# Optimization experiments

Hardware: AMD Instinct MI355X
Metric: run time of the kernel (lower is better)

Reference implementation:

```python
import jax, jax.numpy as jnp
import numpy as np

DIM = 96
D_STATE = 16
D_CONV = 3
D_INNER = 192   # int(DIM * 2.0)
DT_RANK = 6     # ceil(DIM / 16)
K = 4           # cross-scan directions
BATCH, H, W = 2, 56, 56


def setup_inputs() -> dict:
    key = jax.random.key(0)
    k = jax.random.split(key, 8)
    x = jax.random.normal(k[0], (BATCH, DIM, H, W), jnp.float32)
    W_in = jax.random.normal(k[1], (DIM, 2 * D_INNER), jnp.float32) / np.sqrt(DIM)
    W_conv = jax.random.normal(k[2], (D_INNER, 1, D_CONV, D_CONV), jnp.float32) / D_CONV
    b_conv = jnp.zeros((D_INNER,), jnp.float32)
    W_xproj = jax.random.normal(k[3], (K, D_INNER, DT_RANK + 2 * D_STATE), jnp.float32) / np.sqrt(D_INNER)
    W_dt = jax.random.normal(k[4], (K, DT_RANK, D_INNER), jnp.float32) / np.sqrt(DT_RANK)
    # dt bias init as in torch: dt ~ exp(U * (log 0.1 - log 0.001) + log 0.001), inv-softplus
    dt = jnp.exp(jax.random.uniform(k[5], (K, D_INNER), jnp.float32)
                 * (np.log(0.1) - np.log(0.001)) + np.log(0.001))
    dt = jnp.clip(dt, 1e-4, None)
    b_dt = dt + jnp.log(-jnp.expm1(-dt))
    A_logs = jnp.log(jnp.broadcast_to(jnp.arange(1, D_STATE + 1, dtype=jnp.float32),
                                      (K, D_INNER, D_STATE)))
    Ds = jnp.ones((K, D_INNER), jnp.float32)
    W_out = jax.random.normal(k[6], (D_INNER, DIM), jnp.float32) / np.sqrt(D_INNER)
    return dict(x=x, W_in=W_in, W_conv=W_conv, b_conv=b_conv, W_xproj=W_xproj,
                W_dt=W_dt, b_dt=b_dt, A_logs=A_logs, Ds=Ds, W_out=W_out)


def _ss2d(x, W_in, W_conv, b_conv, W_xproj, W_dt, b_dt, A_logs, Ds, W_out):
    Bsz, C, Hh, Ww = x.shape
    L = Hh * Ww
    # in_proj
    xf = x.transpose(0, 2, 3, 1).reshape(Bsz, L, C)        # (B, L, C)
    xz = xf @ W_in
    xp, z = jnp.split(xz, 2, axis=-1)                       # each (B, L, D)
    # depthwise conv + silu
    xi = xp.reshape(Bsz, Hh, Ww, -1).transpose(0, 3, 1, 2)  # (B, D, H, W)
    pad = D_CONV // 2
    xi = jax.lax.conv_general_dilated(
        xi, W_conv, (1, 1), ((pad, pad), (pad, pad)),
        feature_group_count=xi.shape[1],
        dimension_numbers=('NCHW', 'OIHW', 'NCHW')) + b_conv[None, :, None, None]
    xi = jax.nn.silu(xi)
    D = xi.shape[1]
    # cross-scan: 4 directions, each (B, L, D)
    x1 = xi.reshape(Bsz, D, L).transpose(0, 2, 1)
    x2 = xi[:, :, :, ::-1].reshape(Bsz, D, L).transpose(0, 2, 1)
    xt = xi.transpose(0, 1, 3, 2)                           # (B, D, W, H)
    x3 = xt.reshape(Bsz, D, L).transpose(0, 2, 1)
    x4 = xt[:, :, :, ::-1].reshape(Bsz, D, L).transpose(0, 2, 1)
    xs = jnp.stack([x1, x2, x3, x4])                        # (K, B, L, D)
    # per-direction projections, batched over K
    xdbl = jnp.einsum('kbld,kde->kble', xs, W_xproj)
    dr = xdbl[..., :DT_RANK]
    Bk = xdbl[..., DT_RANK:DT_RANK + D_STATE]               # (K, B, L, N)
    Ck = xdbl[..., DT_RANK + D_STATE:]                      # (K, B, L, N)
    delta = jax.nn.softplus(jnp.einsum('kblr,krd->kbld', dr, W_dt)
                            + b_dt[:, None, None, :])       # (K, B, L, D)
    A = -jnp.exp(A_logs)                                    # (K, D, N)

    def step(h, inp):
        x_i, d_i, B_i, C_i = inp  # (K,B,D), (K,B,D), (K,B,N), (K,B,N)
        dA = jnp.exp(d_i[..., None] * A[:, None])           # (K, B, D, N)
        h = dA * h + (d_i * x_i)[..., None] * B_i[:, :, None, :]
        y = jnp.einsum('kbdn,kbn->kbd', h, C_i)
        return h, y

    h0 = jnp.zeros((K, Bsz, D, D_STATE), xs.dtype)
    seq = (xs.transpose(2, 0, 1, 3), delta.transpose(2, 0, 1, 3),
           Bk.transpose(2, 0, 1, 3), Ck.transpose(2, 0, 1, 3))
    _, ys = jax.lax.scan(step, h0, seq)                     # (L, K, B, D)
    ys = ys.transpose(1, 2, 0, 3) + xs * Ds[:, None, None, :]  # (K, B, L, D)
    # cross-merge back to row-major (h w) order
    y1 = ys[0]
    y2 = ys[1].reshape(Bsz, Hh, Ww, D)[:, :, ::-1, :].reshape(Bsz, L, D)
    y3 = ys[2].reshape(Bsz, Ww, Hh, D).transpose(0, 2, 1, 3).reshape(Bsz, L, D)
    y4 = ys[3].reshape(Bsz, Ww, Hh, D)[:, :, ::-1, :].transpose(0, 2, 1, 3).reshape(Bsz, L, D)
    y = (y1 + y2 + y3 + y4) * jax.nn.silu(z)
    out = (y @ W_out).reshape(Bsz, Hh, Ww, C).transpose(0, 3, 1, 2)
    return out


def reference(x, W_in, W_conv, b_conv, W_xproj, W_dt, b_dt, A_logs, Ds, W_out):
    return _ss2d(x, W_in, W_conv, b_conv, W_xproj, W_dt, b_dt, A_logs, Ds, W_out)
```

## Files before the change

kernel.cpp:

```cpp
#include <hip/hip_runtime.h>
#include <math.h>

constexpr int BATCH  = 2;
constexpr int CDIM   = 96;
constexpr int HH     = 56;
constexpr int WW     = 56;
constexpr int LL     = HH * WW;
constexpr int DIN    = 192;
constexpr int NK     = 4;
constexpr int NST    = 16;
constexpr int RNK    = 6;
constexpr int EPROJ  = RNK + 2 * NST;
constexpr int SCH    = 64;
constexpr int NCH    = LL / SCH;
constexpr int CGRP   = DIN / 16;

constexpr size_t SZ_PX   = (size_t)BATCH * LL * DIN;
constexpr size_t OFF_XP  = 0;
constexpr size_t OFF_Z   = OFF_XP + SZ_PX;
constexpr size_t OFF_XI  = OFF_Z  + SZ_PX;
constexpr size_t OFF_DL  = OFF_XI + SZ_PX;
constexpr size_t SZ_DL   = (size_t)NK * BATCH * LL * DIN;
constexpr size_t OFF_B   = OFF_DL + SZ_DL;
constexpr size_t SZ_BC   = (size_t)NK * BATCH * LL * NST;
constexpr size_t OFF_C   = OFF_B + SZ_BC;
constexpr size_t OFF_Y   = OFF_C + SZ_BC;
constexpr size_t SZ_HS   = (size_t)NK * BATCH * NCH * DIN * NST;
constexpr size_t OFF_HE  = OFF_Y + SZ_PX;
constexpr size_t OFF_HI  = OFF_HE + SZ_HS;

__device__ __forceinline__ float silu(float v) {
    return v / (1.0f + __expf(-v));
}

__device__ __forceinline__ float row_reduce16(float p) {
    p += __int_as_float(__builtin_amdgcn_update_dpp(0, __float_as_int(p), 0x128, 0xf, 0xf, true));
    p += __int_as_float(__builtin_amdgcn_update_dpp(0, __float_as_int(p), 0x124, 0xf, 0xf, true));
    p += __int_as_float(__builtin_amdgcn_update_dpp(0, __float_as_int(p), 0x122, 0xf, 0xf, true));
    p += __int_as_float(__builtin_amdgcn_update_dpp(0, __float_as_int(p), 0x121, 0xf, 0xf, true));
    return p;
}

__device__ __forceinline__ int seq_to_lr(int k, int l) {
    int q = l / WW;
    int r = l - q * WW;
    if (k == 0) return l;
    if (k == 1) return q * WW + (WW - 1 - r);
    if (k == 2) return r * WW + q;
    return (WW - 1 - r) * WW + q;
}

__device__ __forceinline__ int spatial_to_seq(int k, int s) {
    int h = s / WW;
    int w = s - h * WW;
    if (k == 0) return s;
    if (k == 1) return h * WW + (WW - 1 - w);
    if (k == 2) return w * WW + h;
    return w * WW + (WW - 1 - h);
}

__device__ __forceinline__ size_t hs_idx(int c, int kb, int d, int n) {
    return ((size_t)(c * (NK * BATCH) + kb) * DIN + d) * NST + n;
}

constexpr int K1_PIX = 8;
__global__ __launch_bounds__(384) void k_inproj(
        const float* __restrict__ x, const float* __restrict__ W_in,
        float* __restrict__ xp, float* __restrict__ z) {
    __shared__ float sx[K1_PIX][100];
    int gp0 = blockIdx.x * K1_PIX;
    int t   = threadIdx.x;
    int b   = gp0 / LL;
    int l0  = gp0 - b * LL;
    for (int i = t; i < K1_PIX * CDIM; i += 384) {
        int p = i % K1_PIX;
        int c = i / K1_PIX;
        sx[p][c] = x[((size_t)(b * CDIM + c)) * LL + l0 + p];
    }
    __syncthreads();
    int e = t;
    float acc[K1_PIX];
#pragma unroll
    for (int p = 0; p < K1_PIX; p++) acc[p] = 0.0f;
    for (int c = 0; c < CDIM; c++) {
        float w = W_in[c * (2 * DIN) + e];
#pragma unroll
        for (int p = 0; p < K1_PIX; p++) acc[p] = fmaf(sx[p][c], w, acc[p]);
    }
    if (e < DIN) {
#pragma unroll
        for (int p = 0; p < K1_PIX; p++)
            xp[((size_t)(gp0 + p)) * DIN + e] = acc[p];
    } else {
        int e2 = e - DIN;
#pragma unroll
        for (int p = 0; p < K1_PIX; p++)
            z[((size_t)(gp0 + p)) * DIN + e2] = acc[p];
    }
}

__global__ __launch_bounds__(192) void k_conv(
        const float* __restrict__ xp, const float* __restrict__ Wc,
        const float* __restrict__ bc, float* __restrict__ xi) {
    int gp = blockIdx.x;
    int d  = threadIdx.x;
    int b  = gp / LL;
    int l  = gp - b * LL;
    int h  = l / WW;
    int w  = l - h * WW;
    float acc = bc[d];
#pragma unroll
    for (int dy = -1; dy <= 1; dy++) {
        int hh = h + dy;
        if (hh < 0 || hh >= HH) continue;
#pragma unroll
        for (int dx = -1; dx <= 1; dx++) {
            int ww = w + dx;
            if (ww < 0 || ww >= WW) continue;
            acc = fmaf(xp[((size_t)b * LL + hh * WW + ww) * DIN + d],
                       Wc[d * 9 + (dy + 1) * 3 + (dx + 1)], acc);
        }
    }
    xi[(size_t)gp * DIN + d] = silu(acc);
}

constexpr int K3_PIX = 16;
__global__ __launch_bounds__(256) void k_xproj(
        const float* __restrict__ xi, const float* __restrict__ W_xproj,
        const float* __restrict__ W_dt, const float* __restrict__ b_dt,
        const float* __restrict__ Ds,
        float* __restrict__ dbuf, float* __restrict__ Bbuf,
        float* __restrict__ Cbuf, float* __restrict__ ysum) {
    __shared__ float v[K3_PIX][DIN];
    __shared__ float drs[K3_PIX][RNK];
    int k   = blockIdx.y;
    int gp0 = blockIdx.x * K3_PIX;
    int b   = gp0 / LL;
    int l0  = gp0 - b * LL;
    int t   = threadIdx.x;
    for (int i = t; i < K3_PIX * DIN; i += 256) {
        int p = i / DIN, d = i % DIN;
        v[p][d] = xi[((size_t)(gp0 + p)) * DIN + d];
    }
    __syncthreads();
    for (int i = t; i < K3_PIX * EPROJ; i += 256) {
        int p = i / EPROJ, e = i % EPROJ;
        const float* wp = W_xproj + (size_t)k * DIN * EPROJ + e;
        float acc = 0.0f;
        for (int d = 0; d < DIN; d++) acc = fmaf(v[p][d], wp[d * EPROJ], acc);
        int ls = spatial_to_seq(k, l0 + p);
        size_t base = ((size_t)(k * BATCH + b)) * LL + ls;
        if (e < RNK)            drs[p][e] = acc;
        else if (e < RNK + NST) Bbuf[base * NST + (e - RNK)] = acc;
        else                    Cbuf[base * NST + (e - RNK - NST)] = acc;
    }
    __syncthreads();
    for (int i = t; i < K3_PIX * DIN; i += 256) {
        int p = i / DIN, d = i % DIN;
        float acc = b_dt[k * DIN + d];
#pragma unroll
        for (int r = 0; r < RNK; r++)
            acc = fmaf(drs[p][r], W_dt[((size_t)k * RNK + r) * DIN + d], acc);
        float sp = (acc > 20.0f) ? acc : log1pf(__expf(acc));
        int ls = spatial_to_seq(k, l0 + p);
        dbuf[(((size_t)(k * BATCH + b)) * LL + ls) * DIN + d] = sp;
        if (k == 0) {
            float dsum = Ds[d] + Ds[DIN + d] + Ds[2 * DIN + d] + Ds[3 * DIN + d];
            ysum[((size_t)(gp0 + p)) * DIN + d] = v[p][d] * dsum;
        }
    }
}

__global__ __launch_bounds__(256) void k_scanA(
        const float* __restrict__ xi, const float* __restrict__ dbuf,
        const float* __restrict__ Bbuf, const float* __restrict__ A_logs,
        float* __restrict__ Pbuf, float* __restrict__ hend) {
    __shared__ float2 sDU[SCH][16];
    __shared__ float  sB1[SCH][16];
    int c   = blockIdx.x;
    int blk = blockIdx.y;
    int k   = blk / (BATCH * CGRP);
    int rem = blk % (BATCH * CGRP);
    int b   = rem / CGRP;
    int cg  = rem % CGRP;
    int d0  = cg * 16;
    int t    = threadIdx.x;
    int lane = t & 63, wave = t >> 6;
    int grp  = lane >> 4, n = lane & 15;
    int ch   = wave * 4 + grp;
    int d    = d0 + ch;
    float A = -__expf(A_logs[((size_t)(k * DIN + d)) * NST + n]);
    size_t sbase = ((size_t)(k * BATCH + b)) * LL;
    const float* dp = dbuf + sbase * DIN + d0;
    const float* bp = Bbuf + sbase * NST;
    const float* up = xi   + (size_t)b * LL * DIN;
    int l0 = c * SCH;
    for (int i = t; i < SCH * 16; i += 256) {
        int s = i >> 4, cc = i & 15;
        int l = l0 + s;
        int lr = seq_to_lr(k, l);
        float dlt = dp[(size_t)l * DIN + cc];
        float u   = up[(size_t)lr * DIN + d0 + cc];
        sDU[s][cc] = make_float2(dlt, dlt * u);
        sB1[s][cc] = bp[(size_t)l * NST + cc];
    }
    __syncthreads();
    float h = 0.0f, P = 1.0f;
#pragma unroll 8
    for (int s = 0; s < SCH; s++) {
        float2 du = sDU[s][ch];
        float dA  = __expf(du.x * A);
        h = fmaf(dA, h, du.y * sB1[s][n]);
        P *= dA;
    }
    size_t idx = hs_idx(c, k * BATCH + b, d, n);
    Pbuf[idx] = P;
    hend[idx] = h;
}

__global__ __launch_bounds__(256) void k_scanB(
        const float* __restrict__ Pbuf, const float* __restrict__ hend,
        float* __restrict__ hin) {
    int tid = blockIdx.x * 256 + threadIdx.x;
    int kb  = tid / (DIN * NST);
    int dn  = tid % (DIN * NST);
    float h = 0.0f;
    for (int c = 0; c < NCH; c++) {
        size_t idx = ((size_t)(c * (NK * BATCH) + kb)) * (DIN * NST) + dn;
        hin[idx] = h;
        h = fmaf(Pbuf[idx], h, hend[idx]);
    }
}

__global__ __launch_bounds__(256) void k_scanC(
        const float* __restrict__ xi, const float* __restrict__ dbuf,
        const float* __restrict__ Bbuf, const float* __restrict__ Cbuf,
        const float* __restrict__ A_logs, const float* __restrict__ hin,
        float* __restrict__ ysum) {
    __shared__ float2 sDU[SCH][16];
    __shared__ float2 sBC[SCH][16];
    __shared__ float  sY[SCH][16];
    int c   = blockIdx.x;
    int blk = blockIdx.y;
    int k   = blk / (BATCH * CGRP);
    int rem = blk % (BATCH * CGRP);
    int b   = rem / CGRP;
    int cg  = rem % CGRP;
    int d0  = cg * 16;
    int t    = threadIdx.x;
    int lane = t & 63, wave = t >> 6;
    int grp  = lane >> 4, n = lane & 15;
    int ch   = wave * 4 + grp;
    int d    = d0 + ch;
    float A = -__expf(A_logs[((size_t)(k * DIN + d)) * NST + n]);
    size_t sbase = ((size_t)(k * BATCH + b)) * LL;
    const float* dp = dbuf + sbase * DIN + d0;
    const float* bp = Bbuf + sbase * NST;
    const float* cp = Cbuf + sbase * NST;
    const float* up = xi   + (size_t)b * LL * DIN;
    float*       yp = ysum + (size_t)b * LL * DIN;
    int l0 = c * SCH;
    for (int i = t; i < SCH * 16; i += 256) {
        int s = i >> 4, cc = i & 15;
        int l = l0 + s;
        int lr = seq_to_lr(k, l);
        float dlt = dp[(size_t)l * DIN + cc];
        float u   = up[(size_t)lr * DIN + d0 + cc];
        sDU[s][cc] = make_float2(dlt, dlt * u);
        sBC[s][cc] = make_float2(bp[(size_t)l * NST + cc],
                                 cp[(size_t)l * NST + cc]);
    }
    float h = hin[hs_idx(c, k * BATCH + b, d, n)];
    __syncthreads();
#pragma unroll 4
    for (int s = 0; s < SCH; s++) {
        float2 du = sDU[s][ch];
        float2 bc = sBC[s][n];
        float dA  = __expf(du.x * A);
        h = fmaf(dA, h, du.y * bc.x);
        float p = row_reduce16(h * bc.y);
        if (n == 0) sY[s][ch] = p;
    }
    __syncthreads();
    for (int i = t; i < SCH * 16; i += 256) {
        int s = i >> 4, cc = i & 15;
        int lr = seq_to_lr(k, l0 + s);
        atomicAdd(&yp[(size_t)lr * DIN + d0 + cc], sY[s][cc]);
    }
}

constexpr int K5_PIX = 8;
__global__ __launch_bounds__(192) void k_out(
        const float* __restrict__ ysum, const float* __restrict__ zbuf,
        const float* __restrict__ W_out, float* __restrict__ out) {
    __shared__ float g[K5_PIX][DIN];
    __shared__ float so[CDIM][K5_PIX];
    int gp0 = blockIdx.x * K5_PIX;
    int b   = gp0 / LL;
    int l0  = gp0 - b * LL;
    int t   = threadIdx.x;
    for (int i = t; i < K5_PIX * DIN; i += 192) {
        int p = i / DIN, dd = i % DIN;
        size_t idx = (size_t)(gp0 + p) * DIN + dd;
        g[p][dd] = ysum[idx] * silu(zbuf[idx]);
    }
    __syncthreads();
    int f    = t % CDIM;
    int half = t / CDIM;
    float acc[4] = {0.f, 0.f, 0.f, 0.f};
    for (int dd = 0; dd < DIN; dd++) {
        float wv = W_out[dd * CDIM + f];
#pragma unroll
        for (int p = 0; p < 4; p++)
            acc[p] = fmaf(g[half * 4 + p][dd], wv, acc[p]);
    }
#pragma unroll
    for (int p = 0; p < 4; p++) so[f][half * 4 + p] = acc[p];
    __syncthreads();
    for (int i = t; i < CDIM * K5_PIX; i += 192) {
        int f2 = i / K5_PIX, p2 = i % K5_PIX;
        out[((size_t)(b * CDIM + f2)) * LL + l0 + p2] = so[f2][p2];
    }
}

extern "C" void kernel_launch(void* const* d_in, const int* in_sizes, int n_in,
                              void* d_out, int out_size, void* d_ws, size_t ws_size,
                              hipStream_t stream) {
    const float* x       = (const float*)d_in[0];
    const float* W_in    = (const float*)d_in[1];
    const float* W_conv  = (const float*)d_in[2];
    const float* b_conv  = (const float*)d_in[3];
    const float* W_xproj = (const float*)d_in[4];
    const float* W_dt    = (const float*)d_in[5];
    const float* b_dt    = (const float*)d_in[6];
    const float* A_logs  = (const float*)d_in[7];
    const float* Ds      = (const float*)d_in[8];
    const float* W_out   = (const float*)d_in[9];
    float* out = (float*)d_out;
    float* ws  = (float*)d_ws;

    float* xp   = ws + OFF_XP;
    float* z    = ws + OFF_Z;
    float* xi   = ws + OFF_XI;
    float* dbuf = ws + OFF_DL;
    float* Bbuf = ws + OFF_B;
    float* Cbuf = ws + OFF_C;
    float* ysum = ws + OFF_Y;
    float* hend = ws + OFF_HE;
    float* hin  = ws + OFF_HI;
    float* Pbuf = xp;

    k_inproj<<<(BATCH * LL) / K1_PIX, 384, 0, stream>>>(x, W_in, xp, z);
    k_conv<<<BATCH * LL, DIN, 0, stream>>>(xp, W_conv, b_conv, xi);
    dim3 g3((BATCH * LL) / K3_PIX, NK);
    k_xproj<<<g3, 256, 0, stream>>>(xi, W_xproj, W_dt, b_dt, Ds, dbuf, Bbuf, Cbuf, ysum);
    dim3 gs(NCH, NK * BATCH * CGRP);
    k_scanA<<<gs, 256, 0, stream>>>(xi, dbuf, Bbuf, A_logs, Pbuf, hend);
    k_scanB<<<(NK * BATCH * DIN * NST) / 256, 256, 0, stream>>>(Pbuf, hend, hin);
    k_scanC<<<gs, 256, 0, stream>>>(xi, dbuf, Bbuf, Cbuf, A_logs, hin, ysum);
    k_out<<<(BATCH * LL) / K5_PIX, 192, 0, stream>>>(ysum, z, W_out, out);
}
```

Before: 244.7 us.

## Recompute delta in scan kernels from low-rank projection instead of materializing it

Instead of writing the full per-direction delta tensor (K*B*L*D floats) in the x-projection kernel, only the rank-6 intermediate is stored, padded to 8 floats per position. Both scan kernels recompute the dt projection and softplus on the fly from this buffer and W_dt. The x-projection is also rewritten to use a transposed weight copy, built by a new small kernel each call, with float4 loads and two outputs per thread. This removes most of the delta write and read traffic, at the cost of recomputing the projection twice and one extra kernel launch.

```diff
diff --git a/kernel.cpp b/kernel.cpp
--- a/kernel.cpp
+++ b/kernel.cpp
@@ -19,18 +19,24 @@
 constexpr size_t OFF_XP  = 0;
 constexpr size_t OFF_Z   = OFF_XP + SZ_PX;
 constexpr size_t OFF_XI  = OFF_Z  + SZ_PX;
-constexpr size_t OFF_DL  = OFF_XI + SZ_PX;
-constexpr size_t SZ_DL   = (size_t)NK * BATCH * LL * DIN;
-constexpr size_t OFF_B   = OFF_DL + SZ_DL;
+constexpr size_t OFF_DR  = OFF_XI + SZ_PX;
+constexpr size_t SZ_DR   = (size_t)NK * BATCH * LL * 8;
+constexpr size_t OFF_B   = OFF_DR + SZ_DR;
 constexpr size_t SZ_BC   = (size_t)NK * BATCH * LL * NST;
 constexpr size_t OFF_C   = OFF_B + SZ_BC;
 constexpr size_t OFF_Y   = OFF_C + SZ_BC;
 constexpr size_t SZ_HS   = (size_t)NK * BATCH * NCH * DIN * NST;
 constexpr size_t OFF_HE  = OFF_Y + SZ_PX;
 constexpr size_t OFF_HI  = OFF_HE + SZ_HS;
+constexpr size_t OFF_WT  = OFF_HI + SZ_HS;
+constexpr size_t SZ_WT   = (size_t)NK * EPROJ * DIN;
 
 __device__ __forceinline__ float silu(float v) {
     return v / (1.0f + __expf(-v));
+}
+
+__device__ __forceinline__ float softplus_f(float x) {
+    return (x > 20.0f) ? x : __logf(1.0f + __expf(x));
 }
 
 __device__ __forceinline__ float row_reduce16(float p) {
@@ -61,6 +67,17 @@
 
 __device__ __forceinline__ size_t hs_idx(int c, int kb, int d, int n) {
     return ((size_t)(c * (NK * BATCH) + kb) * DIN + d) * NST + n;
+}
+
+__global__ __launch_bounds__(256) void k_wt(
+        const float* __restrict__ W_xproj, float* __restrict__ Wt) {
+    int i = blockIdx.x * 256 + threadIdx.x;
+    if (i >= NK * DIN * EPROJ) return;
+    int k = i / (DIN * EPROJ);
+    int r = i % (DIN * EPROJ);
+    int d = r / EPROJ;
+    int e = r % EPROJ;
+    Wt[((size_t)k * EPROJ + e) * DIN + d] = W_xproj[i];
 }
 
 constexpr int K1_PIX = 8;
@@ -126,54 +143,62 @@
 
 constexpr int K3_PIX = 16;
 __global__ __launch_bounds__(256) void k_xproj(
-        const float* __restrict__ xi, const float* __restrict__ W_xproj,
-        const float* __restrict__ W_dt, const float* __restrict__ b_dt,
+        const float* __restrict__ xi, const float* __restrict__ Wt,
         const float* __restrict__ Ds,
-        float* __restrict__ dbuf, float* __restrict__ Bbuf,
+        float* __restrict__ drbuf, float* __restrict__ Bbuf,
         float* __restrict__ Cbuf, float* __restrict__ ysum) {
-    __shared__ float v[K3_PIX][DIN];
-    __shared__ float drs[K3_PIX][RNK];
+    __shared__ float4 sv[K3_PIX][48];
     int k   = blockIdx.y;
     int gp0 = blockIdx.x * K3_PIX;
     int b   = gp0 / LL;
     int l0  = gp0 - b * LL;
     int t   = threadIdx.x;
-    for (int i = t; i < K3_PIX * DIN; i += 256) {
-        int p = i / DIN, d = i % DIN;
-        v[p][d] = xi[((size_t)(gp0 + p)) * DIN + d];
-    }
-    __syncthreads();
-    for (int i = t; i < K3_PIX * EPROJ; i += 256) {
-        int p = i / EPROJ, e = i % EPROJ;
-        const float* wp = W_xproj + (size_t)k * DIN * EPROJ + e;
-        float acc = 0.0f;
-        for (int d = 0; d < DIN; d++) acc = fmaf(v[p][d], wp[d * EPROJ], acc);
+    const float4* xin = (const float4*)(xi + (size_t)gp0 * DIN);
+    for (int i = t; i < K3_PIX * 48; i += 256)
+        sv[i / 48][i % 48] = xin[i];
+    __syncthreads();
+    if (k == 0) {
+        const float* svf = (const float*)sv;
+        for (int i = t; i < K3_PIX * DIN; i += 256) {
+            int d = i % DIN;
+            float dsum = Ds[d] + Ds[DIN + d] + Ds[2 * DIN + d] + Ds[3 * DIN + d];
+            ysum[(size_t)gp0 * DIN + i] = svf[i] * dsum;
+        }
+    }
+    for (int item = t; item < K3_PIX * 19; item += 256) {
+        int p  = item / 19;
+        int e0 = 2 * (item % 19);
+        const float4* w0 = (const float4*)(Wt + ((size_t)k * EPROJ + e0) * DIN);
+        const float4* w1 = w0 + 48;
+        float a0 = 0.0f, a1 = 0.0f;
+#pragma unroll 8
+        for (int j = 0; j < 48; j++) {
+            float4 vv = sv[p][j];
+            float4 wa = w0[j];
+            float4 wb = w1[j];
+            a0 = fmaf(vv.x, wa.x, a0); a0 = fmaf(vv.y, wa.y, a0);
+            a0 = fmaf(vv.z, wa.z, a0); a0 = fmaf(vv.w, wa.w, a0);
+            a1 = fmaf(vv.x, wb.x, a1); a1 = fmaf(vv.y, wb.y, a1);
+            a1 = fmaf(vv.z, wb.z, a1); a1 = fmaf(vv.w, wb.w, a1);
+        }
         int ls = spatial_to_seq(k, l0 + p);
-        size_t base = ((size_t)(k * BATCH + b)) * LL + ls;
-        if (e < RNK)            drs[p][e] = acc;
-        else if (e < RNK + NST) Bbuf[base * NST + (e - RNK)] = acc;
-        else                    Cbuf[base * NST + (e - RNK - NST)] = acc;
-    }
-    __syncthreads();
-    for (int i = t; i < K3_PIX * DIN; i += 256) {
-        int p = i / DIN, d = i % DIN;
-        float acc = b_dt[k * DIN + d];
-#pragma unroll
-        for (int r = 0; r < RNK; r++)
-            acc = fmaf(drs[p][r], W_dt[((size_t)k * RNK + r) * DIN + d], acc);
-        float sp = (acc > 20.0f) ? acc : log1pf(__expf(acc));
-        int ls = spatial_to_seq(k, l0 + p);
-        dbuf[(((size_t)(k * BATCH + b)) * LL + ls) * DIN + d] = sp;
-        if (k == 0) {
-            float dsum = Ds[d] + Ds[DIN + d] + Ds[2 * DIN + d] + Ds[3 * DIN + d];
-            ysum[((size_t)(gp0 + p)) * DIN + d] = v[p][d] * dsum;
+        size_t kb   = (size_t)(k * BATCH + b);
+        size_t b8   = (kb * LL + ls) * 8;
+        size_t b16  = (kb * LL + ls) * NST;
+        if (e0 < RNK) {
+            drbuf[b8 + e0] = a0; drbuf[b8 + e0 + 1] = a1;
+        } else if (e0 < RNK + NST) {
+            Bbuf[b16 + e0 - RNK] = a0; Bbuf[b16 + e0 - RNK + 1] = a1;
+        } else {
+            Cbuf[b16 + e0 - RNK - NST] = a0; Cbuf[b16 + e0 - RNK - NST + 1] = a1;
         }
     }
 }
 
 __global__ __launch_bounds__(256) void k_scanA(
-        const float* __restrict__ xi, const float* __restrict__ dbuf,
+        const float* __restrict__ xi, const float* __restrict__ drbuf,
         const float* __restrict__ Bbuf, const float* __restrict__ A_logs,
+        const float* __restrict__ W_dt, const float* __restrict__ b_dt,
         float* __restrict__ Pbuf, float* __restrict__ hend) {
     __shared__ float2 sDU[SCH][16];
     __shared__ float  sB1[SCH][16];
@@ -190,17 +215,31 @@
     int ch   = wave * 4 + grp;
     int d    = d0 + ch;
     float A = -__expf(A_logs[((size_t)(k * DIN + d)) * NST + n]);
-    size_t sbase = ((size_t)(k * BATCH + b)) * LL;
-    const float* dp = dbuf + sbase * DIN + d0;
-    const float* bp = Bbuf + sbase * NST;
-    const float* up = xi   + (size_t)b * LL * DIN;
+    size_t kb = (size_t)(k * BATCH + b);
+    const float* drp = drbuf + kb * LL * 8;
+    const float* bp  = Bbuf  + kb * LL * NST;
+    const float* up  = xi    + (size_t)b * LL * DIN;
+    int dloc = d0 + (t & 15);
+    float bb = b_dt[k * DIN + dloc];
+    float w0 = W_dt[((size_t)k * RNK + 0) * DIN + dloc];
+    float w1 = W_dt[((size_t)k * RNK + 1) * DIN + dloc];
+    float w2 = W_dt[((size_t)k * RNK + 2) * DIN + dloc];
+    float w3 = W_dt[((size_t)k * RNK + 3) * DIN + dloc];
+    float w4 = W_dt[((size_t)k * RNK + 4) * DIN + dloc];
+    float w5 = W_dt[((size_t)k * RNK + 5) * DIN + dloc];
     int l0 = c * SCH;
     for (int i = t; i < SCH * 16; i += 256) {
         int s = i >> 4, cc = i & 15;
         int l = l0 + s;
         int lr = seq_to_lr(k, l);
-        float dlt = dp[(size_t)l * DIN + cc];
-        float u   = up[(size_t)lr * DIN + d0 + cc];
+        float4 r03 = *(const float4*)(drp + (size_t)l * 8);
+        float2 r45 = *(const float2*)(drp + (size_t)l * 8 + 4);
+        float raw = bb;
+        raw = fmaf(r03.x, w0, raw); raw = fmaf(r03.y, w1, raw);
+        raw = fmaf(r03.z, w2, raw); raw = fmaf(r03.w, w3, raw);
+        raw = fmaf(r45.x, w4, raw); raw = fmaf(r45.y, w5, raw);
+        float dlt = softplus_f(raw);
+        float u = up[(size_t)lr * DIN + d0 + cc];
         sDU[s][cc] = make_float2(dlt, dlt * u);
         sB1[s][cc] = bp[(size_t)l * NST + cc];
     }
@@ -213,7 +252,7 @@
         h = fmaf(dA, h, du.y * sB1[s][n]);
         P *= dA;
     }
-    size_t idx = hs_idx(c, k * BATCH + b, d, n);
+    size_t idx = hs_idx(c, (int)kb, d, n);
     Pbuf[idx] = P;
     hend[idx] = h;
 }
@@ -233,9 +272,10 @@
 }
 
 __global__ __launch_bounds__(256) void k_scanC(
-        const float* __restrict__ xi, const float* __restrict__ dbuf,
+        const float* __restrict__ xi, const float* __restrict__ drbuf,
         const float* __restrict__ Bbuf, const float* __restrict__ Cbuf,
-        const float* __restrict__ A_logs, const float* __restrict__ hin,
+        const float* __restrict__ A_logs, const float* __restrict__ W_dt,
+        const float* __restrict__ b_dt, const float* __restrict__ hin,
         float* __restrict__ ysum) {
     __shared__ float2 sDU[SCH][16];
     __shared__ float2 sBC[SCH][16];
@@ -253,24 +293,38 @@
     int ch   = wave * 4 + grp;
     int d    = d0 + ch;
     float A = -__expf(A_logs[((size_t)(k * DIN + d)) * NST + n]);
-    size_t sbase = ((size_t)(k * BATCH + b)) * LL;
-    const float* dp = dbuf + sbase * DIN + d0;
-    const float* bp = Bbuf + sbase * NST;
-    const float* cp = Cbuf + sbase * NST;
-    const float* up = xi   + (size_t)b * LL * DIN;
-    float*       yp = ysum + (size_t)b * LL * DIN;
+    size_t kb = (size_t)(k * BATCH + b);
+    const float* drp = drbuf + kb * LL * 8;
+    const float* bp  = Bbuf  + kb * LL * NST;
+    const float* cp  = Cbuf  + kb * LL * NST;
+    const float* up  = xi    + (size_t)b * LL * DIN;
+    float*       yp  = ysum  + (size_t)b * LL * DIN;
+    int dloc = d0 + (t & 15);
+    float bb = b_dt[k * DIN + dloc];
+    float w0 = W_dt[((size_t)k * RNK + 0) * DIN + dloc];
+    float w1 = W_dt[((size_t)k * RNK + 1) * DIN + dloc];
+    float w2 = W_dt[((size_t)k * RNK + 2) * DIN + dloc];
+    float w3 = W_dt[((size_t)k * RNK + 3) * DIN + dloc];
+    float w4 = W_dt[((size_t)k * RNK + 4) * DIN + dloc];
+    float w5 = W_dt[((size_t)k * RNK + 5) * DIN + dloc];
     int l0 = c * SCH;
     for (int i = t; i < SCH * 16; i += 256) {
         int s = i >> 4, cc = i & 15;
         int l = l0 + s;
         int lr = seq_to_lr(k, l);
-        float dlt = dp[(size_t)l * DIN + cc];
-        float u   = up[(size_t)lr * DIN + d0 + cc];
+        float4 r03 = *(const float4*)(drp + (size_t)l * 8);
+        float2 r45 = *(const float2*)(drp + (size_t)l * 8 + 4);
+        float raw = bb;
+        raw = fmaf(r03.x, w0, raw); raw = fmaf(r03.y, w1, raw);
+        raw = fmaf(r03.z, w2, raw); raw = fmaf(r03.w, w3, raw);
+        raw = fmaf(r45.x, w4, raw); raw = fmaf(r45.y, w5, raw);
+        float dlt = softplus_f(raw);
+        float u = up[(size_t)lr * DIN + d0 + cc];
         sDU[s][cc] = make_float2(dlt, dlt * u);
         sBC[s][cc] = make_float2(bp[(size_t)l * NST + cc],
                                  cp[(size_t)l * NST + cc]);
     }
-    float h = hin[hs_idx(c, k * BATCH + b, d, n)];
+    float h = hin[hs_idx(c, (int)kb, d, n)];
     __syncthreads();
 #pragma unroll 4
     for (int s = 0; s < SCH; s++) {
@@ -339,24 +393,26 @@
     float* out = (float*)d_out;
     float* ws  = (float*)d_ws;
 
-    float* xp   = ws + OFF_XP;
-    float* z    = ws + OFF_Z;
-    float* xi   = ws + OFF_XI;
-    float* dbuf = ws + OFF_DL;
-    float* Bbuf = ws + OFF_B;
-    float* Cbuf = ws + OFF_C;
-    float* ysum = ws + OFF_Y;
-    float* hend = ws + OFF_HE;
-    float* hin  = ws + OFF_HI;
-    float* Pbuf = xp;
-
+    float* xp    = ws + OFF_XP;
+    float* z     = ws + OFF_Z;
+    float* xi    = ws + OFF_XI;
+    float* drbuf = ws + OFF_DR;
+    float* Bbuf  = ws + OFF_B;
+    float* Cbuf  = ws + OFF_C;
+    float* ysum  = ws + OFF_Y;
+    float* hend  = ws + OFF_HE;
+    float* hin   = ws + OFF_HI;
+    float* Wt    = ws + OFF_WT;
+    float* Pbuf  = xp;
+
+    k_wt<<<(NK * DIN * EPROJ + 255) / 256, 256, 0, stream>>>(W_xproj, Wt);
     k_inproj<<<(BATCH * LL) / K1_PIX, 384, 0, stream>>>(x, W_in, xp, z);
     k_conv<<<BATCH * LL, DIN, 0, stream>>>(xp, W_conv, b_conv, xi);
     dim3 g3((BATCH * LL) / K3_PIX, NK);
-    k_xproj<<<g3, 256, 0, stream>>>(xi, W_xproj, W_dt, b_dt, Ds, dbuf, Bbuf, Cbuf, ysum);
+    k_xproj<<<g3, 256, 0, stream>>>(xi, Wt, Ds, drbuf, Bbuf, Cbuf, ysum);
     dim3 gs(NCH, NK * BATCH * CGRP);
-    k_scanA<<<gs, 256, 0, stream>>>(xi, dbuf, Bbuf, A_logs, Pbuf, hend);
+    k_scanA<<<gs, 256, 0, stream>>>(xi, drbuf, Bbuf, A_logs, W_dt, b_dt, Pbuf, hend);
     k_scanB<<<(NK * BATCH * DIN * NST) / 256, 256, 0, stream>>>(Pbuf, hend, hin);
-    k_scanC<<<gs, 256, 0, stream>>>(xi, dbuf, Bbuf, Cbuf, A_logs, hin, ysum);
+    k_scanC<<<gs, 256, 0, stream>>>(xi, drbuf, Bbuf, Cbuf, A_logs, W_dt, b_dt, hin, ysum);
     k_out<<<(BATCH * LL) / K5_PIX, 192, 0, stream>>>(ysum, z, W_out, out);
 }
```

After: 277.8 us. 1.14x slower.
